# Kernel optimization log

Measured on AMD Instinct MI355X. Metric: run time of the kernel, lower is better.

## Reference

```python
import jax, jax.numpy as jnp
import numpy as np

N = 4096          # num_nodes
E = 131072        # num_edges (avg degree 32)
H = 32            # hidden_channels
C_IN, C_OUT = 3, 3
DEPTH = 4
KS = [2000, 1000, 500, 250]  # ceil(ratio * n) per level, ratios = [2000/N, .5, .5, .5]


def gcn(x, A, W, b):
    """GCNConv with improved=True (self-loop fill 2, preserved if already present),
    symmetric normalization, aggregation out[dst] += norm * h[src]."""
    d = jnp.diagonal(A)
    A_hat = A + jnp.diag(jnp.where(d > 0, 0.0, 2.0))
    deg = A_hat.sum(0)                       # in-degree (col sums), as gcn_norm
    dis = jnp.where(deg > 0, jax.lax.rsqrt(deg), 0.0)
    msg = (x @ W) * dis[:, None]
    return (A_hat.T @ msg) * dis[:, None] + b


def augment(A):
    """GraphUNet.augment_adj: add self loops (w=1), square adjacency, drop self loops."""
    n = A.shape[0]
    eye = jnp.eye(n, dtype=A.dtype)
    A_sl = A + eye
    return (A_sl @ A_sl) * (1.0 - eye)


def pool(x, A, p, k):
    """TopKPooling: score = tanh((x.p)/||p||), keep top-k, gate x by score."""
    score = jnp.tanh((x @ p) / jnp.linalg.norm(p))
    vals, perm = jax.lax.top_k(score, k)
    return x[perm] * vals[:, None], A[perm][:, perm], perm


def setup_inputs() -> dict:
    key = jax.random.key(0)
    ks = jax.random.split(key, 12)
    x = jax.random.normal(ks[0], (N, C_IN), jnp.float32)
    edge_index = jax.random.randint(ks[1], (2, E), 0, N, dtype=jnp.int64)
    s = 0.1
    return {
        "x": x,
        "edge_index": edge_index,
        "W0": jax.random.normal(ks[2], (C_IN, H)) * s,
        "b0": jnp.zeros((H,), jnp.float32),
        "Wd": jax.random.normal(ks[3], (DEPTH, H, H)) * s,
        "bd": jnp.zeros((DEPTH, H), jnp.float32),
        "P": jax.random.normal(ks[4], (DEPTH, H)) * s,
        "Wu": jax.random.normal(ks[5], (DEPTH - 1, H, H)) * s,
        "bu": jnp.zeros((DEPTH - 1, H), jnp.float32),
        "Wlast": jax.random.normal(ks[6], (H, C_OUT)) * s,
        "blast": jnp.zeros((C_OUT,), jnp.float32),
    }


def reference(x, edge_index, W0, b0, Wd, bd, P, Wu, bu, Wlast, blast):
    # dense adjacency; duplicate edges accumulate like coalesced sparse weights
    A = jnp.zeros((N, N), jnp.float32).at[edge_index[0], edge_index[1]].add(1.0)
    x = jax.nn.relu(gcn(x, A, W0, b0))
    xs, As, perms = [x], [A], []
    for i in range(DEPTH):
        A = augment(A)
        x, A, perm = pool(x, A, P[i], KS[i])
        x = jax.nn.relu(gcn(x, A, Wd[i], bd[i]))
        if i < DEPTH - 1:
            xs.append(x)
            As.append(A)
        perms.append(perm)
    for i in range(DEPTH):
        j = DEPTH - 1 - i
        res = xs[j]
        up = jnp.zeros_like(res).at[perms[j]].set(x)  # unpool
        x = res + up                                   # sum_res=True
        if i < DEPTH - 1:
            x = jax.nn.relu(gcn(x, As[j], Wu[i], bu[i]))
        else:
            x = gcn(x, As[j], Wlast, blast)
    return jax.nn.log_softmax(x, axis=1)
```

## Files before the change

kernel.cpp:

```cpp
#include <hip/hip_runtime.h>
#include <math.h>

#define H 32
#define N0 4096
#define EMAX 131072
#define APSTR (4096 * 32)

typedef __attribute__((ext_vector_type(4))) float floatx4;
typedef __attribute__((ext_vector_type(8))) short short8;

__device__ __forceinline__ unsigned short f2bf_bits(float v) {
    union { float f; unsigned u; } c;
    c.f = v;
    unsigned lsb = (c.u >> 16) & 1u;
    c.u += 0x7fffu + lsb;
    return (unsigned short)(c.u >> 16);
}

__global__ void fill_sentinel_kernel(float* out, int n) {
    int t = blockIdx.x * 256 + threadIdx.x;
    if (t < n) out[t] = 9.0f;
}

__global__ void build_stats_kernel(const int* __restrict__ ei, int E, int* __restrict__ rowcnt,
                                   int* __restrict__ rowcntD, int* __restrict__ diagcnt) {
    int t = blockIdx.x * 256 + threadIdx.x;
    if (t >= E) return;
    int s = ei[t], d = ei[E + t];
    if ((unsigned)s >= N0 || (unsigned)d >= N0) return;
    atomicAdd(&rowcnt[s], 1);
    atomicAdd(&rowcntD[d], 1);
    if (s == d) atomicAdd(&diagcnt[s], 1);
}

__global__ __launch_bounds__(1024) void scan2_kernel(const int* __restrict__ cntA, int* __restrict__ rowpA,
                                                     int* __restrict__ curA, const int* __restrict__ cntB,
                                                     int* __restrict__ rowpB, int* __restrict__ curB) {
    __shared__ int part[1024];
    int tid = threadIdx.x;
    for (int pass = 0; pass < 2; pass++) {
        const int* cnt = pass ? cntB : cntA;
        int* rowp = pass ? rowpB : rowpA;
        int* cur = pass ? curB : curA;
        int base = tid * 4;
        int local[4];
        int s = 0;
#pragma unroll
        for (int i = 0; i < 4; i++) { local[i] = s; s += cnt[base + i]; }
        part[tid] = s;
        __syncthreads();
        for (int off = 1; off < 1024; off <<= 1) {
            int v = (tid >= off) ? part[tid - off] : 0;
            __syncthreads();
            part[tid] += v;
            __syncthreads();
        }
        int pre = (tid == 0) ? 0 : part[tid - 1];
#pragma unroll
        for (int i = 0; i < 4; i++) { rowp[base + i] = pre + local[i]; cur[base + i] = pre + local[i]; }
        if (tid == 1023) rowp[N0] = pre + s;
        __syncthreads();
    }
}

__global__ void fillcsr_msg0_kernel(const int* __restrict__ ei, int E, int* __restrict__ cursor,
                                    int* __restrict__ cols, int* __restrict__ cursorD,
                                    int* __restrict__ srcs, const float* __restrict__ x,
                                    const float* __restrict__ Wb, const int* __restrict__ rcntD,
                                    const int* __restrict__ diagcnt, float* __restrict__ dis,
                                    float* __restrict__ fixb, float* __restrict__ msg, int n) {
    int nf = (E + 255) >> 8;
    int tid = threadIdx.x;
    if ((int)blockIdx.x < nf) {
        int t = blockIdx.x * 256 + tid;
        if (t >= E) return;
        int s = ei[t], d = ei[E + t];
        if ((unsigned)s >= N0 || (unsigned)d >= N0) return;
        int pos = atomicAdd(&cursor[s], 1);
        cols[pos] = d;
        int posD = atomicAdd(&cursorD[d], 1);
        srcs[posD] = s;
    } else {
        int idx = ((int)blockIdx.x - nf) * 256 + tid;
        if (idx >= n * 32) return;
        int i = idx >> 5, c = idx & 31;
        float fx = diagcnt[i] > 0 ? 0.f : 2.f;
        float dg = (float)rcntD[i] + fx;
        float di = dg > 0.f ? 1.f / sqrtf(dg) : 0.f;
        if (c == 0) { dis[i] = di; fixb[i] = fx; }
        float s = x[i * 3] * Wb[c] + x[i * 3 + 1] * Wb[32 + c] + x[i * 3 + 2] * Wb[64 + c];
        msg[idx] = s * di;
    }
}

__global__ __launch_bounds__(256) void aug0_kernel(const int* __restrict__ rowp, const int* __restrict__ cols,
                                                   const int* __restrict__ perm, const int* __restrict__ invperm,
                                                   int kOut, int ldC, float* __restrict__ C) {
    __shared__ float row[2048];
    int a = blockIdx.x;
    int tid = threadIdx.x;
    for (int j = tid; j < ldC; j += 256) row[j] = 0.f;
    __syncthreads();
    if (a < kOut) {
        int pa = perm[a];
        int s0 = rowp[pa], s1 = rowp[pa + 1];
        int sub = tid & 7, grp = tid >> 3;
        for (int e = s0 + grp; e < s1; e += 32) {
            int k = cols[e];
            if (sub == 0) {
                int ip = invperm[k];
                if (ip >= 0) atomicAdd(&row[ip], 2.0f);
            }
            int t1 = rowp[k + 1];
            for (int e2 = rowp[k] + sub; e2 < t1; e2 += 8) {
                int ip2 = invperm[cols[e2]];
                if (ip2 >= 0) atomicAdd(&row[ip2], 1.0f);
            }
        }
    }
    __syncthreads();
    for (int j = tid; j < ldC; j += 256) C[(long)a * ldC + j] = (j == a) ? 0.f : row[j];
}

__global__ void gatherAB_bf16_kernel(const float* __restrict__ M, int ldM, const int* __restrict__ perm,
                                     const int* __restrict__ invp, int kOut,
                                     unsigned short* __restrict__ Gr,
                                     unsigned short* __restrict__ GcT, int ldn,
                                     float* __restrict__ Cz) {
    __shared__ float t[32][33];
    __shared__ int rj[32];
    int half = (ldM >> 8) * ldn;
    int tseg = (ldM >> 5) * (ldM >> 5);
    int zrow = (((ldn - kOut) * ldM) + 255) >> 8;
    int u = blockIdx.x;
    int tid = threadIdx.x;
    if (u < half) {
        int gx = ldM >> 8;
        int a = u / gx;
        int k = (u % gx) * 256 + tid;
        float v = 0.f;
        if (a < kOut) {
            int pa = perm[a];
            v = M[(long)pa * ldM + k] + (k == pa ? 1.f : 0.f);
        }
        Gr[(long)a * ldM + k] = f2bf_bits(v);
    } else if (u < half + tseg) {
        u -= half;
        int ntx = ldM >> 5;
        int bx = u % ntx, by = u / ntx;
        int j0 = bx * 32, k0 = by * 32;
        int tx = tid & 31, ty = tid >> 5;
        if (ty == 0) rj[tx] = invp[j0 + tx];
        __syncthreads();
        for (int y = ty; y < 32; y += 8)
            t[y][tx] = M[(long)(k0 + y) * ldM + j0 + tx];
        __syncthreads();
        for (int y = ty; y < 32; y += 8) {
            int r = rj[y];
            if (r >= 0)
                GcT[(long)r * ldM + k0 + tx] =
                    f2bf_bits(t[tx][y] + ((k0 + tx) == (j0 + y) ? 1.f : 0.f));
        }
    } else if (u < half + tseg + zrow) {
        int e = (u - half - tseg) * 256 + tid;
        if (e < (ldn - kOut) * ldM) GcT[(long)kOut * ldM + e] = 0;
    } else {
        int t4 = (u - half - tseg - zrow) * 256 + tid;
        if (t4 < (ldn * ldn) >> 2) {
            floatx4 z = {0.f, 0.f, 0.f, 0.f};
            ((floatx4*)Cz)[t4] = z;
        }
    }
}

__global__ void gatherGT_kernel(const float* __restrict__ M, int ldM, const int* __restrict__ perm,
                                const int* __restrict__ invp, int kOut,
                                float* __restrict__ Gr, float* __restrict__ GcT, int ldn,
                                float* __restrict__ deg) {
    __shared__ float t[32][33];
    __shared__ int rj[32];
    int half = (ldM >> 8) * ldn;
    int tseg = (ldM >> 5) * (ldM >> 5);
    int zrow = (((ldn - kOut) * ldM) + 255) >> 8;
    int u = blockIdx.x;
    int tid = threadIdx.x;
    if (u < half) {
        int gx = ldM >> 8;
        int a = u / gx;
        int k = (u % gx) * 256 + tid;
        float v = 0.f;
        if (a < kOut) {
            int pa = perm[a];
            v = M[(long)pa * ldM + k] + (k == pa ? 1.f : 0.f);
        }
        Gr[(long)a * ldM + k] = v;
    } else if (u < half + tseg) {
        u -= half;
        int ntx = ldM >> 5;
        int bx = u % ntx, by = u / ntx;
        int j0 = bx * 32, k0 = by * 32;
        int tx = tid & 31, ty = tid >> 5;
        if (ty == 0) rj[tx] = invp[j0 + tx];
        __syncthreads();
        for (int y = ty; y < 32; y += 8)
            t[y][tx] = M[(long)(k0 + y) * ldM + j0 + tx];
        __syncthreads();
        for (int y = ty; y < 32; y += 8) {
            int r = rj[y];
            if (r >= 0)
                GcT[(long)r * ldM + k0 + tx] = t[tx][y] + ((k0 + tx) == (j0 + y) ? 1.f : 0.f);
        }
    } else if (u < half + tseg + zrow) {
        int e = (u - half - tseg) * 256 + tid;
        if (e < (ldn - kOut) * ldM) GcT[(long)kOut * ldM + e] = 0.f;
    } else {
        int tt = (u - half - tseg - zrow) * 256 + tid;
        if (tt < ldn) deg[tt] = 0.f;
    }
}

__global__ __launch_bounds__(256) void mfma_aug_kernel(const unsigned short* __restrict__ Aop,
                                                       const unsigned short* __restrict__ Bop,
                                                       float* __restrict__ C, int K, int ldC, int kchunk) {
    __shared__ __align__(16) unsigned short lA[64 * 32];
    __shared__ __align__(16) unsigned short lB[64 * 32];
    const int tid = threadIdx.x;
    const int lane = tid & 63;
    const int w = tid >> 6;
    const int a0 = blockIdx.y * 64, b0 = blockIdx.x * 64;
    const int kbase = blockIdx.z * kchunk;
    const int r0 = tid >> 2;
    const int c8 = (tid & 3) * 8;
    const unsigned short* gA = Aop + (long)(a0 + r0) * K + kbase + c8;
    const unsigned short* gB = Bop + (long)(b0 + r0) * K + kbase + c8;
    const int wm = (w & 1) * 32;
    const int wn = (w >> 1) * 32;
    const int lm = lane & 15;
    const int quad = lane >> 4;
    floatx4 acc[2][2];
#pragma unroll
    for (int i = 0; i < 2; i++)
#pragma unroll
        for (int j = 0; j < 2; j++) {
            floatx4 z = {0.f, 0.f, 0.f, 0.f};
            acc[i][j] = z;
        }
    for (int k0 = 0; k0 < kchunk; k0 += 32) {
        short8 va = *(const short8*)(gA + k0);
        short8 vb = *(const short8*)(gB + k0);
        __syncthreads();
        *(short8*)&lA[r0 * 32 + c8] = va;
        *(short8*)&lB[r0 * 32 + c8] = vb;
        __syncthreads();
        short8 af[2], bf[2];
#pragma unroll
        for (int mi = 0; mi < 2; mi++) af[mi] = *(const short8*)&lA[(wm + mi * 16 + lm) * 32 + quad * 8];
#pragma unroll
        for (int ni = 0; ni < 2; ni++) bf[ni] = *(const short8*)&lB[(wn + ni * 16 + lm) * 32 + quad * 8];
#pragma unroll
        for (int mi = 0; mi < 2; mi++)
#pragma unroll
            for (int ni = 0; ni < 2; ni++)
                acc[mi][ni] = __builtin_amdgcn_mfma_f32_16x16x32_bf16(af[mi], bf[ni], acc[mi][ni], 0, 0, 0);
    }
#pragma unroll
    for (int mi = 0; mi < 2; mi++)
#pragma unroll
        for (int ni = 0; ni < 2; ni++) {
            int col = b0 + wn + ni * 16 + lm;
#pragma unroll
            for (int r = 0; r < 4; r++) {
                int row = a0 + wm + mi * 16 + quad * 4 + r;
                if (row != col) atomicAdd(&C[(long)row * ldC + col], acc[mi][ni][r]);
            }
        }
}

__global__ __launch_bounds__(256) void gemm64_kernel(const float* __restrict__ Gr,
                                                     const float* __restrict__ GcT,
                                                     float* __restrict__ Cpart, int K, int ldC, int kchunk) {
    __shared__ float As[32][68];
    __shared__ float Bs[32][68];
    const int tid = threadIdx.x;
    const int a0 = blockIdx.y * 64, b0 = blockIdx.x * 64;
    const int kbase = blockIdx.z * kchunk;
    float* Cz = Cpart + (long)blockIdx.z * ldC * ldC;
    const int tx = tid & 15, ty = tid >> 4;
    const int lr = tid >> 2;
    const int lk = (tid & 3) * 8;
    const float* gA = Gr + (long)(a0 + lr) * K + lk + kbase;
    const float* gB = GcT + (long)(b0 + lr) * K + lk + kbase;
    float acc[4][4];
#pragma unroll
    for (int i = 0; i < 4; i++)
#pragma unroll
        for (int j = 0; j < 4; j++) acc[i][j] = 0.f;
    for (int k0 = 0; k0 < kchunk; k0 += 32) {
        float a8[8], b8[8];
#pragma unroll
        for (int i = 0; i < 8; i++) a8[i] = gA[k0 + i];
#pragma unroll
        for (int i = 0; i < 8; i++) b8[i] = gB[k0 + i];
        __syncthreads();
#pragma unroll
        for (int i = 0; i < 8; i++) As[lk + i][lr] = a8[i];
#pragma unroll
        for (int i = 0; i < 8; i++) Bs[lk + i][lr] = b8[i];
        __syncthreads();
#pragma unroll
        for (int k = 0; k < 32; k++) {
            floatx4 av = *(const floatx4*)&As[k][ty * 4];
            floatx4 bv = *(const floatx4*)&Bs[k][tx * 4];
#pragma unroll
            for (int i = 0; i < 4; i++)
#pragma unroll
                for (int j = 0; j < 4; j++) acc[i][j] += av[i] * bv[j];
        }
    }
#pragma unroll
    for (int i = 0; i < 4; i++)
#pragma unroll
        for (int j = 0; j < 4; j++) {
            int a = a0 + ty * 4 + i, b = b0 + tx * 4 + j;
            Cz[(long)a * ldC + b] = acc[i][j];
        }
}

__global__ void reduce_part_deg_kernel(const float* __restrict__ Cpart, float* __restrict__ C,
                                       int ldC, int ksplit, float* __restrict__ deg) {
    int t = blockIdx.x * 256 + threadIdx.x;
    long tot = (long)ldC * ldC;
    if (t >= tot) return;
    float s = 0.f;
    for (int z = 0; z < ksplit; z++) s += Cpart[(long)z * tot + t];
    int a = t / ldC, b = t % ldC;
    if (a == b) s = 0.f;
    C[t] = s;
    if (s != 0.f) atomicAdd(&deg[b], s);
}

__global__ void colsum_rawmsg_kernel(const float* __restrict__ A, int ld, int hascs,
                                     const float* __restrict__ x, const int* __restrict__ perm,
                                     const float* __restrict__ vals, const float* __restrict__ xup,
                                     const int* __restrict__ invp, const float* __restrict__ Wb,
                                     float* __restrict__ degp, float* __restrict__ rm, int n) {
    int nc = hascs ? (ld >> 8) * (ld >> 6) : 0;
    int tid = threadIdx.x;
    if ((int)blockIdx.x < nc) {
        int gx = ld >> 8;
        int bi = blockIdx.x % gx, jb = blockIdx.x / gx;
        int i = bi * 256 + tid;
        int j0 = jb * 64;
        const float* p = A + (long)j0 * ld + i;
        float s0 = 0.f, s1 = 0.f, s2 = 0.f, s3 = 0.f, s4 = 0.f, s5 = 0.f, s6 = 0.f, s7 = 0.f;
#pragma unroll
        for (int jq = 0; jq < 64; jq += 8) {
            float v[8];
#pragma unroll
            for (int q = 0; q < 8; q++) v[q] = p[(long)(jq + q) * ld];
            s0 += v[0]; s1 += v[1]; s2 += v[2]; s3 += v[3];
            s4 += v[4]; s5 += v[5]; s6 += v[6]; s7 += v[7];
        }
        float s = ((s0 + s1) + (s2 + s3)) + ((s4 + s5) + (s6 + s7));
        degp[(long)jb * ld + i] = s;
    } else {
        int idx = ((int)blockIdx.x - nc) * 256 + tid;
        if (idx >= ld * 32) return;
        int i = idx >> 5, c = idx & 31;
        float v = 0.f;
        if (i < n) {
            int src = perm ? perm[i] : i;
            float vs = vals ? vals[i] : 1.f;
            int ip = invp ? invp[i] : -1;
            float s = 0.f;
#pragma unroll
            for (int q = 0; q < 32; q++) {
                float xv = x[(long)src * 32 + q];
                if (ip >= 0) xv += xup[(long)ip * 32 + q];
                s += xv * Wb[q * 32 + c];
            }
            v = s * vs;
        }
        rm[idx] = v;
    }
}

__global__ __launch_bounds__(256) void aggTs_kernel(const float* __restrict__ A,
                                                    const float* __restrict__ rm,
                                                    const float* __restrict__ degp, int nparts,
                                                    const float* __restrict__ disC,
                                                    float* __restrict__ aggp, int n, int ld, int jchunk) {
    __shared__ float As[64][64];
    __shared__ float Ms[64][32];
    __shared__ float sdisJ[256];
    const int tid = threadIdx.x;
    const int i0 = blockIdx.x * 64;
    const int j0 = blockIdx.y * jchunk;
    for (int j = tid; j < jchunk; j += 256) {
        int jj = j0 + j;
        float d;
        if (nparts) {
            float s = 0.f;
            for (int z = 0; z < nparts; z++) s += degp[(long)z * ld + jj];
            d = 1.f / sqrtf(s + 2.f);
        } else {
            d = disC[jj];
        }
        sdisJ[j] = d;
    }
    __syncthreads();
    const int il = tid & 63;
    const int cg = tid >> 6;
    const int i = i0 + il;
    const int mrow = tid >> 2;
    const int mc = (tid & 3) * 8;
    float acc[8];
#pragma unroll
    for (int q = 0; q < 8; q++) acc[q] = 0.f;
    for (int jb = j0; jb < j0 + jchunk; jb += 64) {
        float a16[16], m8[8];
#pragma unroll
        for (int q = 0; q < 16; q++) a16[q] = A[(long)(jb + cg + 4 * q) * ld + i0 + il];
#pragma unroll
        for (int q = 0; q < 8; q++) m8[q] = rm[(long)(jb + mrow) * 32 + mc + q];
        __syncthreads();
#pragma unroll
        for (int q = 0; q < 16; q++) As[cg + 4 * q][il] = a16[q];
        float ds = sdisJ[jb - j0 + mrow];
#pragma unroll
        for (int q = 0; q < 8; q++) Ms[mrow][mc + q] = m8[q] * ds;
        __syncthreads();
#pragma unroll
        for (int jl = 0; jl < 64; jl++) {
            float a = As[jl][il];
#pragma unroll
            for (int q = 0; q < 8; q++) acc[q] += a * Ms[jl][cg * 8 + q];
        }
        __syncthreads();
    }
    if (i < n) {
#pragma unroll
        for (int q = 0; q < 8; q++) aggp[(long)blockIdx.y * APSTR + (long)i * 32 + cg * 8 + q] = acc[q];
    }
}

__global__ void epi2_kernel(const float* __restrict__ aggp, int jsplit, const float* __restrict__ rm,
                            const float* __restrict__ degp, int nparts, float* __restrict__ disC,
                            int writeDis, int ld, const float* __restrict__ bb,
                            float* __restrict__ out, int n, const float* __restrict__ p, int npow,
                            unsigned long long* __restrict__ keys) {
    __shared__ float psh[32];
    if (p) {
        if (threadIdx.x < 32) psh[threadIdx.x] = p[threadIdx.x];
        __syncthreads();
    }
    int idx = blockIdx.x * 256 + threadIdx.x;
    int tot = (p ? npow : n) * 32;
    if (idx >= tot) return;
    int i = idx >> 5, c = idx & 31;
    float di;
    if (nparts) {
        float s = 0.f;
        for (int z = 0; z < nparts; z++) s += degp[(long)z * ld + i];
        di = 1.f / sqrtf(s + 2.f);
    } else {
        di = disC[i];
    }
    float v = 0.f;
    if (i < n) {
        float s = 0.f;
        for (int z = 0; z < jsplit; z++) s += aggp[(long)z * APSTR + idx];
        v = (s + 2.f * di * rm[idx]) * di + bb[c];
        v = fmaxf(v, 0.f);
        out[idx] = v;
    }
    if (writeDis && c == 0) disC[i] = di;
    if (p) {
        float pc = psh[c];
        float d = v * pc;
        float nq = pc * pc;
#pragma unroll
        for (int st = 16; st >= 1; st >>= 1) {
            d += __shfl_xor(d, st);
            nq += __shfl_xor(nq, st);
        }
        if (c == 0) {
            unsigned long long kk = 0ULL;
            if (i < n) {
                float sc = tanhf(d / sqrtf(nq));
                unsigned u = __float_as_uint(sc);
                u = (u & 0x80000000u) ? ~u : (u | 0x80000000u);
                kk = ((unsigned long long)u << 32) | (unsigned)(~i);
            }
            keys[i] = kk;
        }
    }
}

__global__ void cscagg_epi_keys_kernel(const int* __restrict__ rowpD, const int* __restrict__ srcs,
                                       const float* __restrict__ msg, const float* __restrict__ dis,
                                       const float* __restrict__ fixb, const float* __restrict__ bb,
                                       float* __restrict__ out, int n, const float* __restrict__ p,
                                       unsigned long long* __restrict__ keys) {
    __shared__ float psh[32];
    if (threadIdx.x < 32) psh[threadIdx.x] = p[threadIdx.x];
    __syncthreads();
    int idx = blockIdx.x * 256 + threadIdx.x;
    if (idx >= n * 32) return;
    int i = idx >> 5, c = idx & 31;
    float acc = 0.f;
    int e0 = rowpD[i], e1 = rowpD[i + 1];
    for (int e = e0; e < e1; e++) acc += msg[(long)srcs[e] * 32 + c];
    float v = (acc + fixb[i] * msg[idx]) * dis[i] + bb[c];
    v = fmaxf(v, 0.f);
    out[idx] = v;
    float pc = psh[c];
    float d = v * pc;
    float nq = pc * pc;
#pragma unroll
    for (int st = 16; st >= 1; st >>= 1) {
        d += __shfl_xor(d, st);
        nq += __shfl_xor(nq, st);
    }
    if (c == 0) {
        float sc = tanhf(d / sqrtf(nq));
        unsigned u = __float_as_uint(sc);
        u = (u & 0x80000000u) ? ~u : (u | 0x80000000u);
        keys[i] = ((unsigned long long)u << 32) | (unsigned)(~i);
    }
}

__global__ void msg3up_kernel(const float* __restrict__ res, const float* __restrict__ xup,
                              const int* __restrict__ invp, const float* __restrict__ Wb,
                              const float* __restrict__ dis, float* __restrict__ msg, int n) {
    int idx = blockIdx.x * 256 + threadIdx.x;
    if (idx >= n * 3) return;
    int i = idx / 3, c = idx % 3;
    int ip = invp[i];
    float s = 0.f;
#pragma unroll
    for (int q = 0; q < 32; q++) {
        float xv = res[(long)i * 32 + q];
        if (ip >= 0) xv += xup[(long)ip * 32 + q];
        s += xv * Wb[q * 3 + c];
    }
    msg[idx] = s * dis[i];
}

__global__ void cscagg_lsm_kernel(const int* __restrict__ rowpD, const int* __restrict__ srcs,
                                  const float* __restrict__ msg, const float* __restrict__ dis,
                                  const float* __restrict__ fixb, const float* __restrict__ bb,
                                  float* __restrict__ out, int n) {
    int i = blockIdx.x * 256 + threadIdx.x;
    if (i >= n) return;
    float a0 = 0.f, a1 = 0.f, a2 = 0.f;
    int e0 = rowpD[i], e1 = rowpD[i + 1];
    for (int e = e0; e < e1; e++) {
        const float* m = &msg[(long)srcs[e] * 3];
        a0 += m[0]; a1 += m[1]; a2 += m[2];
    }
    float di = dis[i], fx = fixb[i];
    float v0 = (a0 + fx * msg[i * 3]) * di + bb[0];
    float v1 = (a1 + fx * msg[i * 3 + 1]) * di + bb[1];
    float v2 = (a2 + fx * msg[i * 3 + 2]) * di + bb[2];
    float m = fmaxf(v0, fmaxf(v1, v2));
    float s = expf(v0 - m) + expf(v1 - m) + expf(v2 - m);
    float l = m + logf(s);
    out[i * 3] = v0 - l;
    out[i * 3 + 1] = v1 - l;
    out[i * 3 + 2] = v2 - l;
}

__global__ __launch_bounds__(256) void topk_rank_kernel(const unsigned long long* __restrict__ keys,
                                                        int npow, int k, int* __restrict__ perm,
                                                        float* __restrict__ vals,
                                                        int* __restrict__ invperm) {
    __shared__ unsigned long long ks[4096];
    __shared__ int psum[256];
    const int tid = threadIdx.x;
    for (int t = tid; t < npow; t += 256) ks[t] = keys[t];
    __syncthreads();
    const int m = tid & 15;
    const int chunk = tid >> 4;
    const int myi = blockIdx.x * 16 + m;
    unsigned long long my = ks[myi];
    const int cl = npow >> 4;
    const unsigned long long* base = &ks[chunk * cl];
    int r = 0;
#pragma unroll 4
    for (int j = 0; j < cl; j++) r += (base[j] > my) ? 1 : 0;
    psum[chunk * 16 + m] = r;
    __syncthreads();
    if (tid < 16) {
        int mk_i = blockIdx.x * 16 + tid;
        unsigned long long mk = ks[mk_i];
        int rank = 0;
#pragma unroll
        for (int c = 0; c < 16; c++) rank += psum[c * 16 + tid];
        invperm[mk_i] = (rank < k) ? rank : -1;
        if (rank < k) {
            perm[rank] = (int)(~(unsigned)mk);
            unsigned u = (unsigned)(mk >> 32);
            u = (u & 0x80000000u) ? (u ^ 0x80000000u) : ~u;
            vals[rank] = __uint_as_float(u);
        }
    }
}

static void run_dense(hipStream_t st, const float* A, int n, int ld, const float* x,
                      const int* perm, const float* vals, const float* xup, const int* invp,
                      const float* Wt, const float* bt, float* out,
                      float* degp, int nparts, int hascs, float* disC, int writeDis,
                      float* aggp, float* rm,
                      const float* pnext, int npow, unsigned long long* keys) {
    {
        int nc = hascs ? (ld >> 8) * (ld >> 6) : 0;
        int g = nc + (ld * 32 + 255) / 256;
        colsum_rawmsg_kernel<<<g, 256, 0, st>>>(A, ld, hascs, x, perm, vals, xup, invp, Wt,
                                                degp, rm, n);
    }
    int jsplit = (ld >= 256) ? (ld >> 8) : 1;
    if (jsplit < 1) jsplit = 1;
    int jchunk = ld / jsplit;
    dim3 ga(ld / 64, jsplit);
    aggTs_kernel<<<ga, 256, 0, st>>>(A, rm, nparts ? degp : nullptr, nparts, disC, aggp, n, ld,
                                     jchunk);
    int gme = ((pnext ? npow : n) * 32 + 255) / 256;
    epi2_kernel<<<gme, 256, 0, st>>>(aggp, jsplit, rm, nparts ? degp : nullptr, nparts, disC,
                                     writeDis, ld, bt, out, n, pnext, npow, keys);
}

extern "C" void kernel_launch(void* const* d_in, const int* in_sizes, int n_in,
                              void* d_out, int out_size, void* d_ws, size_t ws_size,
                              hipStream_t stream) {
    const float* x0f = (const float*)d_in[0];
    const int* eidx = (const int*)d_in[1];
    const float* W0f = (const float*)d_in[2];
    const float* b0f = (const float*)d_in[3];
    const float* Wdf = (const float*)d_in[4];
    const float* bdf = (const float*)d_in[5];
    const float* Pf = (const float*)d_in[6];
    const float* Wuf = (const float*)d_in[7];
    const float* buf2 = (const float*)d_in[8];
    const float* Wlf = (const float*)d_in[9];
    const float* blf = (const float*)d_in[10];
    const int E = in_sizes[1] / 2;

    unsigned char* w = (unsigned char*)d_ws;
    size_t off = 0;
    auto alloc = [&](size_t bytes) -> void* {
        void* p = w + off;
        off += (bytes + 255) & ~(size_t)255;
        return p;
    };
    int* rowcnt = (int*)alloc(N0 * 4);
    int* rowcntD = (int*)alloc(N0 * 4);
    int* diagcnt = (int*)alloc(N0 * 4);
    int* rowp = (int*)alloc((N0 + 1) * 4);
    int* rowpD = (int*)alloc((N0 + 1) * 4);
    int* cursor = (int*)alloc(N0 * 4);
    int* cursorD = (int*)alloc(N0 * 4);
    int* cols = (int*)alloc((size_t)EMAX * 4);
    int* srcs = (int*)alloc((size_t)EMAX * 4);
    float* dis0 = (float*)alloc(N0 * 4);
    float* fixb0 = (float*)alloc(N0 * 4);
    unsigned long long* keys = (unsigned long long*)alloc((size_t)N0 * 8);
    float* A1 = (float*)alloc((size_t)2048 * 2048 * 4);
    float* A2 = (float*)alloc((size_t)1024 * 1024 * 4);
    float* A3 = (float*)alloc((size_t)512 * 512 * 4);
    float* A4 = (float*)alloc((size_t)256 * 256 * 4);
    float* Gr = (float*)alloc((size_t)1024 * 2048 * 4);
    float* Gc = (float*)alloc((size_t)2048 * 1024 * 4);
    unsigned short* Grb = (unsigned short*)alloc((size_t)1024 * 2048 * 2);
    unsigned short* GcTb = (unsigned short*)alloc((size_t)1024 * 2048 * 2);
    float* Cpart = (float*)alloc((size_t)8 * 512 * 512 * 4);
    float* degp = (float*)alloc((size_t)32 * 2048 * 4);
    float* aggp = (float*)alloc((size_t)8 * APSTR * 4);
    float* xs0 = (float*)alloc((size_t)N0 * H * 4);
    float* xs1 = (float*)alloc((size_t)2000 * H * 4);
    float* xs2 = (float*)alloc((size_t)1000 * H * 4);
    float* xs3 = (float*)alloc((size_t)500 * H * 4);
    float* xtB = (float*)alloc((size_t)N0 * H * 4);
    float* xtC = (float*)alloc((size_t)N0 * H * 4);
    float* msgb = (float*)alloc((size_t)N0 * H * 4);
    float* disL = (float*)alloc((size_t)4 * N0 * 4);
    int* invpermL = (int*)alloc((size_t)4 * N0 * 4);
    const int ksz[4] = {2000, 1000, 500, 250};
    int* perm[4];
    float* vals[4];
    for (int i = 0; i < 4; i++) perm[i] = (int*)alloc((size_t)ksz[i] * 4);
    for (int i = 0; i < 4; i++) vals[i] = (float*)alloc((size_t)ksz[i] * 4);

    if (off > ws_size) {
        fill_sentinel_kernel<<<(out_size + 255) / 256, 256, 0, stream>>>((float*)d_out, out_size);
        return;
    }

    const int nlvl[5] = {N0, 2000, 1000, 500, 250};
    const int ldl[5] = {N0, 2048, 1024, 512, 256};
    const int npw[4] = {4096, 2048, 1024, 512};
    float* Afp[5] = {nullptr, A1, A2, A3, A4};
    float* xsb[4] = {xs0, xs1, xs2, xs3};

    hipMemsetAsync(rowcnt, 0, (size_t)N0 * 3 * 4, stream);
    build_stats_kernel<<<(E + 255) / 256, 256, 0, stream>>>(eidx, E, rowcnt, rowcntD, diagcnt);
    scan2_kernel<<<1, 1024, 0, stream>>>(rowcnt, rowp, cursor, rowcntD, rowpD, cursorD);
    {
        int nf = (E + 255) / 256;
        int nm = (N0 * H + 255) / 256;
        fillcsr_msg0_kernel<<<nf + nm, 256, 0, stream>>>(eidx, E, cursor, cols, cursorD, srcs,
                                                         x0f, W0f, rowcntD, diagcnt, dis0, fixb0,
                                                         msgb, N0);
    }
    cscagg_epi_keys_kernel<<<(N0 * H + 255) / 256, 256, 0, stream>>>(rowpD, srcs, msgb, dis0, fixb0,
                                                                     b0f, xs0, N0, Pf, keys);
    float* xcur = xs0;

    for (int i = 0; i < 4; ++i) {
        int kk = ksz[i], ldn = ldl[i + 1];
        topk_rank_kernel<<<npw[i] / 16, 256, 0, stream>>>(keys, npw[i], kk, perm[i], vals[i],
                                                          invpermL + i * N0);
        if (i == 0) {
            aug0_kernel<<<ldn, 256, 0, stream>>>(rowp, cols, perm[0], invpermL, kk, ldn, A1);
        } else if (i == 1) {
            int ldM = ldl[i];
            int half = (ldM >> 8) * ldn;
            int tseg = (ldM >> 5) * (ldM >> 5);
            int zrow = (((ldn - kk) * ldM) + 255) >> 8;
            int zseg = ((ldn * ldn) / 4 + 255) / 256;
            gatherAB_bf16_kernel<<<half + tseg + zrow + zseg, 256, 0, stream>>>(
                Afp[i], ldM, perm[i], invpermL + i * N0, kk, Grb, GcTb, ldn, Afp[i + 1]);
            int ksplit = 4;
            int kchunk = ldM / ksplit;
            dim3 gg(ldn / 64, ldn / 64, ksplit);
            mfma_aug_kernel<<<gg, 256, 0, stream>>>(Grb, GcTb, Afp[i + 1], ldM, ldn, kchunk);
        } else {
            int ldM = ldl[i];
            int half = (ldM >> 8) * ldn;
            int tseg = (ldM >> 5) * (ldM >> 5);
            int zrow = (((ldn - kk) * ldM) + 255) >> 8;
            int dseg = (ldn + 255) / 256;
            gatherGT_kernel<<<half + tseg + zrow + dseg, 256, 0, stream>>>(
                Afp[i], ldM, perm[i], invpermL + i * N0, kk, Gr, Gc, ldn, degp);
            int ksplit = 8;
            int kchunk = ldM / ksplit;
            dim3 gg(ldn / 64, ldn / 64, ksplit);
            gemm64_kernel<<<gg, 256, 0, stream>>>(Gr, Gc, Cpart, ldM, ldn, kchunk);
            long tot = (long)ldn * ldn;
            reduce_part_deg_kernel<<<(tot + 255) / 256, 256, 0, stream>>>(Cpart, Afp[i + 1], ldn,
                                                                          ksplit, degp);
        }
        float* outx = (i < 3) ? xsb[i + 1] : xtB;
        const float* pnext = (i < 3) ? (Pf + (i + 1) * H) : nullptr;
        int npown = (i < 3) ? npw[i + 1] : 0;
        int hascs = (i <= 1) ? 1 : 0;
        int nparts = (i <= 1) ? (ldn >> 6) : 1;
        run_dense(stream, Afp[i + 1], kk, ldn, xcur, perm[i], vals[i], nullptr, nullptr,
                  Wdf + i * (H * H), bdf + i * H, outx, degp, nparts, hascs, disL + i * N0,
                  (i < 3) ? 1 : 0, aggp, msgb, pnext, npown, keys);
        xcur = outx;
    }

    for (int i = 0; i < 4; ++i) {
        int j = 3 - i;
        int nj = nlvl[j];
        if (i < 3) {
            int ldn = ldl[j];
            float* outx = (xcur == xtB) ? xtC : xtB;
            run_dense(stream, Afp[j], nj, ldn, xsb[j], nullptr, nullptr, xcur, invpermL + j * N0,
                      Wuf + i * (H * H), buf2 + i * H, outx, nullptr, 0, 0, disL + (j - 1) * N0, 0,
                      aggp, msgb, nullptr, 0, nullptr);
            xcur = outx;
        } else {
            msg3up_kernel<<<(N0 * 3 + 255) / 256, 256, 0, stream>>>(xs0, xcur, invpermL, Wlf, dis0,
                                                                    msgb, N0);
            cscagg_lsm_kernel<<<(N0 + 255) / 256, 256, 0, stream>>>(rowpD, srcs, msgb, dis0, fixb0,
                                                                    blf, (float*)d_out, N0);
        }
    }
}
```

Measured before the change: 428.1 us.

## Store level-1 adjacency in bf16, rewrite scan with wave shuffles, halve MFMA ksplit

The 2048x2048 level-1 adjacency is now stored as bf16 instead of fp32. The gather, column-sum and aggregation kernels that read it are templated to convert on load, which halves the memory traffic for that matrix across several kernels. Edge counts that are small integers stay exact in bf16, but larger augmented-adjacency counts may round once they exceed 256. The prefix-scan kernel is also rewritten to use wavefront shuffles in a single pass over both arrays, and the MFMA augmentation k-split drops from 4 to 2.

```diff
diff --git a/kernel.cpp b/kernel.cpp
--- a/kernel.cpp
+++ b/kernel.cpp
@@ -16,6 +16,15 @@
     c.u += 0x7fffu + lsb;
     return (unsigned short)(c.u >> 16);
 }
+
+__device__ __forceinline__ float bf2f(unsigned short u) {
+    union { unsigned x; float f; } c;
+    c.x = (unsigned)u << 16;
+    return c.f;
+}
+
+__device__ __forceinline__ float cvtA(float f) { return f; }
+__device__ __forceinline__ float cvtA(unsigned short u) { return bf2f(u); }
 
 __global__ void fill_sentinel_kernel(float* out, int n) {
     int t = blockIdx.x * 256 + threadIdx.x;
@@ -36,31 +45,47 @@
 __global__ __launch_bounds__(1024) void scan2_kernel(const int* __restrict__ cntA, int* __restrict__ rowpA,
                                                      int* __restrict__ curA, const int* __restrict__ cntB,
                                                      int* __restrict__ rowpB, int* __restrict__ curB) {
-    __shared__ int part[1024];
+    __shared__ int wsA[16], wsB[16], weA[16], weB[16];
     int tid = threadIdx.x;
-    for (int pass = 0; pass < 2; pass++) {
-        const int* cnt = pass ? cntB : cntA;
-        int* rowp = pass ? rowpB : rowpA;
-        int* cur = pass ? curB : curA;
-        int base = tid * 4;
-        int local[4];
-        int s = 0;
-#pragma unroll
-        for (int i = 0; i < 4; i++) { local[i] = s; s += cnt[base + i]; }
-        part[tid] = s;
-        __syncthreads();
-        for (int off = 1; off < 1024; off <<= 1) {
-            int v = (tid >= off) ? part[tid - off] : 0;
-            __syncthreads();
-            part[tid] += v;
-            __syncthreads();
-        }
-        int pre = (tid == 0) ? 0 : part[tid - 1];
-#pragma unroll
-        for (int i = 0; i < 4; i++) { rowp[base + i] = pre + local[i]; cur[base + i] = pre + local[i]; }
-        if (tid == 1023) rowp[N0] = pre + s;
-        __syncthreads();
-    }
+    int lane = tid & 63, wid = tid >> 6;
+    int base = tid * 4;
+    int lA[4], lB[4];
+    int sA = 0, sB = 0;
+#pragma unroll
+    for (int i = 0; i < 4; i++) { lA[i] = sA; sA += cntA[base + i]; }
+#pragma unroll
+    for (int i = 0; i < 4; i++) { lB[i] = sB; sB += cntB[base + i]; }
+    int iA = sA, iB = sB;
+#pragma unroll
+    for (int off = 1; off < 64; off <<= 1) {
+        int vA = __shfl_up(iA, off);
+        int vB = __shfl_up(iB, off);
+        if (lane >= off) { iA += vA; iB += vB; }
+    }
+    if (lane == 63) { wsA[wid] = iA; wsB[wid] = iB; }
+    __syncthreads();
+    if (tid < 16) {
+        int a = wsA[tid], b = wsB[tid];
+        int ia = a, ib = b;
+#pragma unroll
+        for (int off = 1; off < 16; off <<= 1) {
+            int va = __shfl_up(ia, off);
+            int vb = __shfl_up(ib, off);
+            if (tid >= off) { ia += va; ib += vb; }
+        }
+        weA[tid] = ia - a;
+        weB[tid] = ib - b;
+    }
+    __syncthreads();
+    int preA = weA[wid] + iA - sA;
+    int preB = weB[wid] + iB - sB;
+#pragma unroll
+    for (int i = 0; i < 4; i++) {
+        int a = preA + lA[i], b = preB + lB[i];
+        rowpA[base + i] = a; curA[base + i] = a;
+        rowpB[base + i] = b; curB[base + i] = b;
+    }
+    if (tid == 1023) { rowpA[N0] = preA + sA; rowpB[N0] = preB + sB; }
 }
 
 __global__ void fillcsr_msg0_kernel(const int* __restrict__ ei, int E, int* __restrict__ cursor,
@@ -95,7 +120,7 @@
 
 __global__ __launch_bounds__(256) void aug0_kernel(const int* __restrict__ rowp, const int* __restrict__ cols,
                                                    const int* __restrict__ perm, const int* __restrict__ invperm,
-                                                   int kOut, int ldC, float* __restrict__ C) {
+                                                   int kOut, int ldC, unsigned short* __restrict__ C) {
     __shared__ float row[2048];
     int a = blockIdx.x;
     int tid = threadIdx.x;
@@ -119,12 +144,13 @@
         }
     }
     __syncthreads();
-    for (int j = tid; j < ldC; j += 256) C[(long)a * ldC + j] = (j == a) ? 0.f : row[j];
-}
-
-__global__ void gatherAB_bf16_kernel(const float* __restrict__ M, int ldM, const int* __restrict__ perm,
-                                     const int* __restrict__ invp, int kOut,
-                                     unsigned short* __restrict__ Gr,
+    for (int j = tid; j < ldC; j += 256)
+        C[(long)a * ldC + j] = (j == a) ? 0 : f2bf_bits(row[j]);
+}
+
+__global__ void gatherAB_bf16_kernel(const unsigned short* __restrict__ M, int ldM,
+                                     const int* __restrict__ perm, const int* __restrict__ invp,
+                                     int kOut, unsigned short* __restrict__ Gr,
                                      unsigned short* __restrict__ GcT, int ldn,
                                      float* __restrict__ Cz) {
     __shared__ float t[32][33];
@@ -141,7 +167,7 @@
         float v = 0.f;
         if (a < kOut) {
             int pa = perm[a];
-            v = M[(long)pa * ldM + k] + (k == pa ? 1.f : 0.f);
+            v = bf2f(M[(long)pa * ldM + k]) + (k == pa ? 1.f : 0.f);
         }
         Gr[(long)a * ldM + k] = f2bf_bits(v);
     } else if (u < half + tseg) {
@@ -153,7 +179,7 @@
         if (ty == 0) rj[tx] = invp[j0 + tx];
         __syncthreads();
         for (int y = ty; y < 32; y += 8)
-            t[y][tx] = M[(long)(k0 + y) * ldM + j0 + tx];
+            t[y][tx] = bf2f(M[(long)(k0 + y) * ldM + j0 + tx]);
         __syncthreads();
         for (int y = ty; y < 32; y += 8) {
             int r = rj[y];
@@ -339,7 +365,8 @@
     if (s != 0.f) atomicAdd(&deg[b], s);
 }
 
-__global__ void colsum_rawmsg_kernel(const float* __restrict__ A, int ld, int hascs,
+template <typename AT>
+__global__ void colsum_rawmsg_kernel(const AT* __restrict__ A, int ld, int hascs,
                                      const float* __restrict__ x, const int* __restrict__ perm,
                                      const float* __restrict__ vals, const float* __restrict__ xup,
                                      const int* __restrict__ invp, const float* __restrict__ Wb,
@@ -351,13 +378,13 @@
         int bi = blockIdx.x % gx, jb = blockIdx.x / gx;
         int i = bi * 256 + tid;
         int j0 = jb * 64;
-        const float* p = A + (long)j0 * ld + i;
+        const AT* p = A + (long)j0 * ld + i;
         float s0 = 0.f, s1 = 0.f, s2 = 0.f, s3 = 0.f, s4 = 0.f, s5 = 0.f, s6 = 0.f, s7 = 0.f;
 #pragma unroll
         for (int jq = 0; jq < 64; jq += 8) {
             float v[8];
 #pragma unroll
-            for (int q = 0; q < 8; q++) v[q] = p[(long)(jq + q) * ld];
+            for (int q = 0; q < 8; q++) v[q] = cvtA(p[(long)(jq + q) * ld]);
             s0 += v[0]; s1 += v[1]; s2 += v[2]; s3 += v[3];
             s4 += v[4]; s5 += v[5]; s6 += v[6]; s7 += v[7];
         }
@@ -385,7 +412,8 @@
     }
 }
 
-__global__ __launch_bounds__(256) void aggTs_kernel(const float* __restrict__ A,
+template <typename AT>
+__global__ __launch_bounds__(256) void aggTs_kernel(const AT* __restrict__ A,
                                                     const float* __restrict__ rm,
                                                     const float* __restrict__ degp, int nparts,
                                                     const float* __restrict__ disC,
@@ -418,14 +446,15 @@
 #pragma unroll
     for (int q = 0; q < 8; q++) acc[q] = 0.f;
     for (int jb = j0; jb < j0 + jchunk; jb += 64) {
-        float a16[16], m8[8];
+        AT a16[16];
+        float m8[8];
 #pragma unroll
         for (int q = 0; q < 16; q++) a16[q] = A[(long)(jb + cg + 4 * q) * ld + i0 + il];
 #pragma unroll
         for (int q = 0; q < 8; q++) m8[q] = rm[(long)(jb + mrow) * 32 + mc + q];
         __syncthreads();
 #pragma unroll
-        for (int q = 0; q < 16; q++) As[cg + 4 * q][il] = a16[q];
+        for (int q = 0; q < 16; q++) As[cg + 4 * q][il] = cvtA(a16[q]);
         float ds = sdisJ[jb - j0 + mrow];
 #pragma unroll
         for (int q = 0; q < 8; q++) Ms[mrow][mc + q] = m8[q] * ds;
@@ -607,7 +636,7 @@
     }
 }
 
-static void run_dense(hipStream_t st, const float* A, int n, int ld, const float* x,
+static void run_dense(hipStream_t st, const void* A, int abf, int n, int ld, const float* x,
                       const int* perm, const float* vals, const float* xup, const int* invp,
                       const float* Wt, const float* bt, float* out,
                       float* degp, int nparts, int hascs, float* disC, int writeDis,
@@ -616,15 +645,24 @@
     {
         int nc = hascs ? (ld >> 8) * (ld >> 6) : 0;
         int g = nc + (ld * 32 + 255) / 256;
-        colsum_rawmsg_kernel<<<g, 256, 0, st>>>(A, ld, hascs, x, perm, vals, xup, invp, Wt,
-                                                degp, rm, n);
+        if (abf)
+            colsum_rawmsg_kernel<unsigned short><<<g, 256, 0, st>>>(
+                (const unsigned short*)A, ld, hascs, x, perm, vals, xup, invp, Wt, degp, rm, n);
+        else
+            colsum_rawmsg_kernel<float><<<g, 256, 0, st>>>(
+                (const float*)A, ld, hascs, x, perm, vals, xup, invp, Wt, degp, rm, n);
     }
     int jsplit = (ld >= 256) ? (ld >> 8) : 1;
     if (jsplit < 1) jsplit = 1;
     int jchunk = ld / jsplit;
     dim3 ga(ld / 64, jsplit);
-    aggTs_kernel<<<ga, 256, 0, st>>>(A, rm, nparts ? degp : nullptr, nparts, disC, aggp, n, ld,
-                                     jchunk);
+    if (abf)
+        aggTs_kernel<unsigned short><<<ga, 256, 0, st>>>((const unsigned short*)A, rm,
+                                                         nparts ? degp : nullptr, nparts, disC,
+                                                         aggp, n, ld, jchunk);
+    else
+        aggTs_kernel<float><<<ga, 256, 0, st>>>((const float*)A, rm, nparts ? degp : nullptr,
+                                                nparts, disC, aggp, n, ld, jchunk);
     int gme = ((pnext ? npow : n) * 32 + 255) / 256;
     epi2_kernel<<<gme, 256, 0, st>>>(aggp, jsplit, rm, nparts ? degp : nullptr, nparts, disC,
                                      writeDis, ld, bt, out, n, pnext, npow, keys);
@@ -665,7 +703,7 @@
     float* dis0 = (float*)alloc(N0 * 4);
     float* fixb0 = (float*)alloc(N0 * 4);
     unsigned long long* keys = (unsigned long long*)alloc((size_t)N0 * 8);
-    float* A1 = (float*)alloc((size_t)2048 * 2048 * 4);
+    unsigned short* A1 = (unsigned short*)alloc((size_t)2048 * 2048 * 2);
     float* A2 = (float*)alloc((size_t)1024 * 1024 * 4);
     float* A3 = (float*)alloc((size_t)512 * 512 * 4);
     float* A4 = (float*)alloc((size_t)256 * 256 * 4);
@@ -699,7 +737,8 @@
     const int nlvl[5] = {N0, 2000, 1000, 500, 250};
     const int ldl[5] = {N0, 2048, 1024, 512, 256};
     const int npw[4] = {4096, 2048, 1024, 512};
-    float* Afp[5] = {nullptr, A1, A2, A3, A4};
+    void* Afp[5] = {nullptr, A1, A2, A3, A4};
+    const int abfL[5] = {0, 1, 0, 0, 0};
     float* xsb[4] = {xs0, xs1, xs2, xs3};
 
     hipMemsetAsync(rowcnt, 0, (size_t)N0 * 3 * 4, stream);
@@ -729,11 +768,11 @@
             int zrow = (((ldn - kk) * ldM) + 255) >> 8;
             int zseg = ((ldn * ldn) / 4 + 255) / 256;
             gatherAB_bf16_kernel<<<half + tseg + zrow + zseg, 256, 0, stream>>>(
-                Afp[i], ldM, perm[i], invpermL + i * N0, kk, Grb, GcTb, ldn, Afp[i + 1]);
-            int ksplit = 4;
+                A1, ldM, perm[i], invpermL + i * N0, kk, Grb, GcTb, ldn, A2);
+            int ksplit = 2;
             int kchunk = ldM / ksplit;
             dim3 gg(ldn / 64, ldn / 64, ksplit);
-            mfma_aug_kernel<<<gg, 256, 0, stream>>>(Grb, GcTb, Afp[i + 1], ldM, ldn, kchunk);
+            mfma_aug_kernel<<<gg, 256, 0, stream>>>(Grb, GcTb, A2, ldM, ldn, kchunk);
         } else {
             int ldM = ldl[i];
             int half = (ldM >> 8) * ldn;
@@ -741,23 +780,23 @@
             int zrow = (((ldn - kk) * ldM) + 255) >> 8;
             int dseg = (ldn + 255) / 256;
             gatherGT_kernel<<<half + tseg + zrow + dseg, 256, 0, stream>>>(
-                Afp[i], ldM, perm[i], invpermL + i * N0, kk, Gr, Gc, ldn, degp);
+                (const float*)Afp[i], ldM, perm[i], invpermL + i * N0, kk, Gr, Gc, ldn, degp);
             int ksplit = 8;
             int kchunk = ldM / ksplit;
             dim3 gg(ldn / 64, ldn / 64, ksplit);
             gemm64_kernel<<<gg, 256, 0, stream>>>(Gr, Gc, Cpart, ldM, ldn, kchunk);
             long tot = (long)ldn * ldn;
-            reduce_part_deg_kernel<<<(tot + 255) / 256, 256, 0, stream>>>(Cpart, Afp[i + 1], ldn,
-                                                                          ksplit, degp);
+            reduce_part_deg_kernel<<<(tot + 255) / 256, 256, 0, stream>>>(Cpart, (float*)Afp[i + 1],
+                                                                          ldn, ksplit, degp);
         }
         float* outx = (i < 3) ? xsb[i + 1] : xtB;
         const float* pnext = (i < 3) ? (Pf + (i + 1) * H) : nullptr;
         int npown = (i < 3) ? npw[i + 1] : 0;
         int hascs = (i <= 1) ? 1 : 0;
         int nparts = (i <= 1) ? (ldn >> 6) : 1;
-        run_dense(stream, Afp[i + 1], kk, ldn, xcur, perm[i], vals[i], nullptr, nullptr,
-                  Wdf + i * (H * H), bdf + i * H, outx, degp, nparts, hascs, disL + i * N0,
-                  (i < 3) ? 1 : 0, aggp, msgb, pnext, npown, keys);
+        run_dense(stream, Afp[i + 1], abfL[i + 1], kk, ldn, xcur, perm[i], vals[i], nullptr,
+                  nullptr, Wdf + i * (H * H), bdf + i * H, outx, degp, nparts, hascs,
+                  disL + i * N0, (i < 3) ? 1 : 0, aggp, msgb, pnext, npown, keys);
         xcur = outx;
     }
 
@@ -767,9 +806,9 @@
         if (i < 3) {
             int ldn = ldl[j];
             float* outx = (xcur == xtB) ? xtC : xtB;
-            run_dense(stream, Afp[j], nj, ldn, xsb[j], nullptr, nullptr, xcur, invpermL + j * N0,
-                      Wuf + i * (H * H), buf2 + i * H, outx, nullptr, 0, 0, disL + (j - 1) * N0, 0,
-                      aggp, msgb, nullptr, 0, nullptr);
+            run_dense(stream, Afp[j], abfL[j], nj, ldn, xsb[j], nullptr, nullptr, xcur,
+                      invpermL + j * N0, Wuf + i * (H * H), buf2 + i * H, outx, nullptr, 0, 0,
+                      disL + (j - 1) * N0, 0, aggp, msgb, nullptr, 0, nullptr);
             xcur = outx;
         } else {
             msg3up_kernel<<<(N0 * 3 + 255) / 256, 256, 0, stream>>>(xs0, xcur, invpermL, Wlf, dis0,
```

New measurement: 421.1 us. Within noise of the previous version (-1.6%).
